# Optimization experiments

Measured on AMD Instinct MI355X. Metric: run time of the kernel, lower is better.

The kernel has to match this reference:

```python
import jax, jax.numpy as jnp
import numpy as np

WAY, SHOT, QUERY = 64, 8, 16


def setup_inputs() -> dict:
    key = jax.random.key(0)
    k1, k2 = jax.random.split(key)
    t, c = 32, 1024
    query_feat = jax.random.normal(k1, (t, WAY * QUERY, c), dtype=jnp.float32)
    support_feat = jax.random.normal(k2, (t, WAY * SHOT, c), dtype=jnp.float32)
    return {"query_feat": query_feat, "support_feat": support_feat}


def reference(query_feat, support_feat):
    t, wq, c = query_feat.shape
    # prototypes: mean over shots -> [t, way, c]
    proto = jnp.mean(support_feat.reshape(t, WAY, SHOT, c), axis=2)
    # squared Euclidean via expansion: ||q||^2 - 2 q.p + ||p||^2
    q_sq = jnp.sum(query_feat * query_feat, axis=-1, keepdims=True)      # [t, wq, 1]
    p_sq = jnp.sum(proto * proto, axis=-1)[:, None, :]                   # [t, 1, way]
    qp = jnp.einsum('tqc,twc->tqw', query_feat, proto)                   # [t, wq, way]
    dist = -(q_sq - 2.0 * qp + p_sq)
    return dist
```

## Files before the change

kernel.cpp:

```cpp
#include <hip/hip_runtime.h>
#include <hip/hip_bf16.h>

#define T 32
#define WAYS 64
#define SHOTS 8
#define CDIM 1024
#define WQ 1024
#define BK 128
#define NK 8

typedef float f32x4 __attribute__((ext_vector_type(4)));
typedef __bf16 bf16x8 __attribute__((ext_vector_type(8)));

__global__ __launch_bounds__(256) void proto_kernel(const float* __restrict__ support,
                                                    __bf16* __restrict__ proto,
                                                    float* __restrict__ p_sq) {
    const int bid = blockIdx.x;
    const int tid = threadIdx.x;
    const float* sp = support + (size_t)bid * (SHOTS * CDIM);
    float4 a = make_float4(0.f, 0.f, 0.f, 0.f);
#pragma unroll
    for (int s = 0; s < SHOTS; ++s) {
        const float4 v = *reinterpret_cast<const float4*>(sp + s * CDIM + tid * 4);
        a.x += v.x; a.y += v.y; a.z += v.z; a.w += v.w;
    }
    a.x *= 0.125f; a.y *= 0.125f; a.z *= 0.125f; a.w *= 0.125f;
    float ps = a.x * a.x + a.y * a.y + a.z * a.z + a.w * a.w;

    union { __bf16 h[4]; uint2 u; } pk;
    pk.h[0] = (__bf16)a.x; pk.h[1] = (__bf16)a.y; pk.h[2] = (__bf16)a.z; pk.h[3] = (__bf16)a.w;
    *reinterpret_cast<uint2*>(proto + (size_t)bid * CDIM + tid * 4) = pk.u;

#pragma unroll
    for (int m = 32; m >= 1; m >>= 1) ps += __shfl_down(ps, m, 64);
    __shared__ float red[4];
    const int wv = tid >> 6, ln = tid & 63;
    if (ln == 0) red[wv] = ps;
    __syncthreads();
    if (tid == 0) p_sq[bid] = red[0] + red[1] + red[2] + red[3];
}

__global__ __launch_bounds__(512, 4) void dist_kernel(const float* __restrict__ query,
                                                      const __bf16* __restrict__ proto,
                                                      const float* __restrict__ p_sq,
                                                      float* __restrict__ out) {
    const int bx = blockIdx.x;
    const int vb = (bx & 7) * 64 + (bx >> 3);
    const int t   = vb >> 4;
    const int mt  = vb & 15;
    const int tid = threadIdx.x;
    const int lane = tid & 63;
    const int wid  = tid >> 6;
    const int wr   = wid >> 1;
    const int wn   = wid & 1;
    const int fr   = lane & 15;
    const int kg   = lane >> 4;

    __shared__ __bf16 As[2][64 * BK];
    __shared__ __bf16 Bs[2][64 * BK];
    __shared__ float qsq_s[64];

    const int srow = tid >> 3;
    const int sk8  = tid & 7;

    const float*  qbase = query + ((size_t)(t * WQ + mt * 64 + srow)) * CDIM + sk8 * 16;
    const __bf16* pbase = proto + ((size_t)(t * WAYS + srow)) * CDIM + sk8 * 16;

    struct Stage { f32x4 a[4]; uint4 b[2]; };

    auto LOAD = [&](int ks) -> Stage {
        Stage s;
        const float* ap = qbase + ks * BK;
#pragma unroll
        for (int p = 0; p < 4; ++p)
            s.a[p] = *reinterpret_cast<const f32x4*>(ap + p * 4);
        const __bf16* bp = pbase + ks * BK;
        s.b[0] = *reinterpret_cast<const uint4*>(bp);
        s.b[1] = *reinterpret_cast<const uint4*>(bp + 8);
        return s;
    };

    float qsq = 0.f;

    auto WRITE = [&](int buf, const Stage& s) {
#pragma unroll
        for (int p = 0; p < 4; ++p)
            qsq += s.a[p].x * s.a[p].x + s.a[p].y * s.a[p].y +
                   s.a[p].z * s.a[p].z + s.a[p].w * s.a[p].w;
        union { __bf16 h[8]; uint4 u; } p0, p1;
#pragma unroll
        for (int j = 0; j < 2; ++j) {
            const f32x4 v0 = s.a[j * 2], v1 = s.a[j * 2 + 1];
            __bf16* h = (j == 0) ? p0.h : p1.h;
            h[0] = (__bf16)v0.x; h[1] = (__bf16)v0.y; h[2] = (__bf16)v0.z; h[3] = (__bf16)v0.w;
            h[4] = (__bf16)v1.x; h[5] = (__bf16)v1.y; h[6] = (__bf16)v1.z; h[7] = (__bf16)v1.w;
        }
        const int swz = (srow & 7) << 4;
        char* ab = reinterpret_cast<char*>(As[buf]);
        *reinterpret_cast<uint4*>(ab + ((srow * 256 + sk8 * 32) ^ swz))      = p0.u;
        *reinterpret_cast<uint4*>(ab + ((srow * 256 + sk8 * 32 + 16) ^ swz)) = p1.u;
        char* bb = reinterpret_cast<char*>(Bs[buf]);
        *reinterpret_cast<uint4*>(bb + ((srow * 256 + sk8 * 32) ^ swz))      = s.b[0];
        *reinterpret_cast<uint4*>(bb + ((srow * 256 + sk8 * 32 + 16) ^ swz)) = s.b[1];
    };

    f32x4 acc[2];
    acc[0] = (f32x4){0.f, 0.f, 0.f, 0.f};
    acc[1] = (f32x4){0.f, 0.f, 0.f, 0.f};

    auto COMPUTE = [&](int buf) {
        const char* ab = reinterpret_cast<const char*>(As[buf]);
        const char* bb = reinterpret_cast<const char*>(Bs[buf]);
#pragma unroll
        for (int ksub = 0; ksub < 4; ++ksub) {
            const int arow = wr * 16 + fr;
            const bf16x8 af = *reinterpret_cast<const bf16x8*>(
                ab + ((arow * 256 + ksub * 64 + kg * 16) ^ ((arow & 7) << 4)));
#pragma unroll
            for (int nf = 0; nf < 2; ++nf) {
                const int way = wn * 32 + nf * 16 + fr;
                const bf16x8 bf = *reinterpret_cast<const bf16x8*>(
                    bb + ((way * 256 + ksub * 64 + kg * 16) ^ ((way & 7) << 4)));
                acc[nf] = __builtin_amdgcn_mfma_f32_16x16x32_bf16(af, bf, acc[nf], 0, 0, 0);
            }
        }
    };

    float psqv[2];
#pragma unroll
    for (int nf = 0; nf < 2; ++nf)
        psqv[nf] = p_sq[t * WAYS + wn * 32 + nf * 16 + fr];

    Stage s0 = LOAD(0);
    Stage sA = LOAD(1);
    WRITE(0, s0);
    asm volatile("s_waitcnt lgkmcnt(0)" ::: "memory");
    __builtin_amdgcn_s_barrier();

#pragma unroll
    for (int ks = 0; ks < NK; ++ks) {
        Stage nx;
        if (ks < NK - 2) nx = LOAD(ks + 2);
        COMPUTE(ks & 1);
        if (ks < NK - 1) WRITE((ks + 1) & 1, sA);
        sA = nx;
        asm volatile("s_waitcnt lgkmcnt(0)" ::: "memory");
        __builtin_amdgcn_s_barrier();
    }

    qsq += __shfl_xor(qsq, 1, 64);
    qsq += __shfl_xor(qsq, 2, 64);
    qsq += __shfl_xor(qsq, 4, 64);
    if (sk8 == 0) qsq_s[srow] = qsq;
    __syncthreads();

    float* ob = out + ((size_t)(t * WQ + mt * 64 + wr * 16)) * WAYS;
#pragma unroll
    for (int r = 0; r < 4; ++r) {
        const int row = kg * 4 + r;
        const float qv = qsq_s[wr * 16 + row];
#pragma unroll
        for (int nf = 0; nf < 2; ++nf) {
            ob[(size_t)row * WAYS + wn * 32 + nf * 16 + fr] =
                2.f * acc[nf][r] - qv - psqv[nf];
        }
    }
}

extern "C" void kernel_launch(void* const* d_in, const int* in_sizes, int n_in,
                              void* d_out, int out_size, void* d_ws, size_t ws_size,
                              hipStream_t stream) {
    const float* query   = (const float*)d_in[0];
    const float* support = (const float*)d_in[1];
    float* out = (float*)d_out;

    __bf16* proto = (__bf16*)d_ws;
    float*  p_sq  = (float*)((char*)d_ws + (size_t)T * WAYS * CDIM * sizeof(__bf16));

    hipLaunchKernelGGL(proto_kernel, dim3(T * WAYS), dim3(256), 0, stream,
                       support, proto, p_sq);
    hipLaunchKernelGGL(dist_kernel, dim3(T * 16), dim3(512), 0, stream,
                       query, proto, p_sq, out);
}
```

Measured before the change: 38.87 us.

## Fuse prototype computation into distance kernel with per-batch atomic counter sync

Merges the prototype-averaging kernel into the distance GEMM kernel. Each of the 16 blocks for a batch index computes 4 prototypes, then bumps an atomic counter. Blocks prefetch their query tiles while tid 0 spins until all 16 producers for that batch have finished. This removes a kernel launch and lets query loads overlap the prototype phase. In exchange it adds a memset and an inter-block spin-wait that relies on all blocks being co-resident; 512 blocks at 4 per CU should fit on the device.

New measurement: 96.22 us. 148% more time.

```diff
diff --git a/kernel.cpp b/kernel.cpp
--- a/kernel.cpp
+++ b/kernel.cpp
@@ -12,38 +12,12 @@
 typedef float f32x4 __attribute__((ext_vector_type(4)));
 typedef __bf16 bf16x8 __attribute__((ext_vector_type(8)));
 
-__global__ __launch_bounds__(256) void proto_kernel(const float* __restrict__ support,
-                                                    __bf16* __restrict__ proto,
-                                                    float* __restrict__ p_sq) {
-    const int bid = blockIdx.x;
-    const int tid = threadIdx.x;
-    const float* sp = support + (size_t)bid * (SHOTS * CDIM);
-    float4 a = make_float4(0.f, 0.f, 0.f, 0.f);
-#pragma unroll
-    for (int s = 0; s < SHOTS; ++s) {
-        const float4 v = *reinterpret_cast<const float4*>(sp + s * CDIM + tid * 4);
-        a.x += v.x; a.y += v.y; a.z += v.z; a.w += v.w;
-    }
-    a.x *= 0.125f; a.y *= 0.125f; a.z *= 0.125f; a.w *= 0.125f;
-    float ps = a.x * a.x + a.y * a.y + a.z * a.z + a.w * a.w;
-
-    union { __bf16 h[4]; uint2 u; } pk;
-    pk.h[0] = (__bf16)a.x; pk.h[1] = (__bf16)a.y; pk.h[2] = (__bf16)a.z; pk.h[3] = (__bf16)a.w;
-    *reinterpret_cast<uint2*>(proto + (size_t)bid * CDIM + tid * 4) = pk.u;
-
-#pragma unroll
-    for (int m = 32; m >= 1; m >>= 1) ps += __shfl_down(ps, m, 64);
-    __shared__ float red[4];
-    const int wv = tid >> 6, ln = tid & 63;
-    if (ln == 0) red[wv] = ps;
-    __syncthreads();
-    if (tid == 0) p_sq[bid] = red[0] + red[1] + red[2] + red[3];
-}
-
-__global__ __launch_bounds__(512, 4) void dist_kernel(const float* __restrict__ query,
-                                                      const __bf16* __restrict__ proto,
-                                                      const float* __restrict__ p_sq,
-                                                      float* __restrict__ out) {
+__global__ __launch_bounds__(512, 4) void fused_kernel(const float* __restrict__ query,
+                                                       const float* __restrict__ support,
+                                                       float* __restrict__ out,
+                                                       __bf16* __restrict__ proto,
+                                                       float* __restrict__ p_sq,
+                                                       int* __restrict__ cnt) {
     const int bx = blockIdx.x;
     const int vb = (bx & 7) * 64 + (bx >> 3);
     const int t   = vb >> 4;
@@ -51,10 +25,49 @@
     const int tid = threadIdx.x;
     const int lane = tid & 63;
     const int wid  = tid >> 6;
-    const int wr   = wid >> 1;
-    const int wn   = wid & 1;
-    const int fr   = lane & 15;
-    const int kg   = lane >> 4;
+
+    __shared__ float redA[8];
+
+    {
+        const int bid = vb * 4 + (wid >> 1);
+        const int ch  = (wid & 1) * 512;
+        const float* sp = support + (size_t)bid * (SHOTS * CDIM) + ch;
+
+        f32x4 a0 = (f32x4){0.f, 0.f, 0.f, 0.f};
+        f32x4 a1 = (f32x4){0.f, 0.f, 0.f, 0.f};
+#pragma unroll
+        for (int s = 0; s < SHOTS; ++s) {
+            a0 += *reinterpret_cast<const f32x4*>(sp + s * CDIM + lane * 4);
+            a1 += *reinterpret_cast<const f32x4*>(sp + s * CDIM + 256 + lane * 4);
+        }
+        a0 *= 0.125f; a1 *= 0.125f;
+        float ps = a0.x * a0.x + a0.y * a0.y + a0.z * a0.z + a0.w * a0.w +
+                   a1.x * a1.x + a1.y * a1.y + a1.z * a1.z + a1.w * a1.w;
+
+        union { __bf16 h[4]; uint2 u; } q0, q1;
+        q0.h[0] = (__bf16)a0.x; q0.h[1] = (__bf16)a0.y;
+        q0.h[2] = (__bf16)a0.z; q0.h[3] = (__bf16)a0.w;
+        q1.h[0] = (__bf16)a1.x; q1.h[1] = (__bf16)a1.y;
+        q1.h[2] = (__bf16)a1.z; q1.h[3] = (__bf16)a1.w;
+        __bf16* pb = proto + (size_t)bid * CDIM + ch;
+        *reinterpret_cast<uint2*>(pb + lane * 4)       = q0.u;
+        *reinterpret_cast<uint2*>(pb + 256 + lane * 4) = q1.u;
+
+#pragma unroll
+        for (int m = 1; m <= 32; m <<= 1) ps += __shfl_xor(ps, m, 64);
+        if (lane == 0) redA[wid] = ps;
+        __syncthreads();
+        if (tid < 4) p_sq[vb * 4 + tid] = redA[2 * tid] + redA[2 * tid + 1];
+        __syncthreads();
+    }
+
+    if (tid == 0)
+        __hip_atomic_fetch_add(&cnt[t], 1, __ATOMIC_RELEASE, __HIP_MEMORY_SCOPE_AGENT);
+
+    const int wr = wid >> 1;
+    const int wn = wid & 1;
+    const int fr = lane & 15;
+    const int kg = lane >> 4;
 
     __shared__ __bf16 As[2][64 * BK];
     __shared__ __bf16 Bs[2][64 * BK];
@@ -66,14 +79,19 @@
     const float*  qbase = query + ((size_t)(t * WQ + mt * 64 + srow)) * CDIM + sk8 * 16;
     const __bf16* pbase = proto + ((size_t)(t * WAYS + srow)) * CDIM + sk8 * 16;
 
-    struct Stage { f32x4 a[4]; uint4 b[2]; };
-
-    auto LOAD = [&](int ks) -> Stage {
-        Stage s;
+    struct StageA { f32x4 a[4]; };
+    struct StageB { uint4 b[2]; };
+
+    auto LOADA = [&](int ks) -> StageA {
+        StageA s;
         const float* ap = qbase + ks * BK;
 #pragma unroll
         for (int p = 0; p < 4; ++p)
             s.a[p] = *reinterpret_cast<const f32x4*>(ap + p * 4);
+        return s;
+    };
+    auto LOADB = [&](int ks) -> StageB {
+        StageB s;
         const __bf16* bp = pbase + ks * BK;
         s.b[0] = *reinterpret_cast<const uint4*>(bp);
         s.b[1] = *reinterpret_cast<const uint4*>(bp + 8);
@@ -82,15 +100,15 @@
 
     float qsq = 0.f;
 
-    auto WRITE = [&](int buf, const Stage& s) {
+    auto WRITE = [&](int buf, const StageA& sa, const StageB& sb) {
 #pragma unroll
         for (int p = 0; p < 4; ++p)
-            qsq += s.a[p].x * s.a[p].x + s.a[p].y * s.a[p].y +
-                   s.a[p].z * s.a[p].z + s.a[p].w * s.a[p].w;
+            qsq += sa.a[p].x * sa.a[p].x + sa.a[p].y * sa.a[p].y +
+                   sa.a[p].z * sa.a[p].z + sa.a[p].w * sa.a[p].w;
         union { __bf16 h[8]; uint4 u; } p0, p1;
 #pragma unroll
         for (int j = 0; j < 2; ++j) {
-            const f32x4 v0 = s.a[j * 2], v1 = s.a[j * 2 + 1];
+            const f32x4 v0 = sa.a[j * 2], v1 = sa.a[j * 2 + 1];
             __bf16* h = (j == 0) ? p0.h : p1.h;
             h[0] = (__bf16)v0.x; h[1] = (__bf16)v0.y; h[2] = (__bf16)v0.z; h[3] = (__bf16)v0.w;
             h[4] = (__bf16)v1.x; h[5] = (__bf16)v1.y; h[6] = (__bf16)v1.z; h[7] = (__bf16)v1.w;
@@ -100,8 +118,8 @@
         *reinterpret_cast<uint4*>(ab + ((srow * 256 + sk8 * 32) ^ swz))      = p0.u;
         *reinterpret_cast<uint4*>(ab + ((srow * 256 + sk8 * 32 + 16) ^ swz)) = p1.u;
         char* bb = reinterpret_cast<char*>(Bs[buf]);
-        *reinterpret_cast<uint4*>(bb + ((srow * 256 + sk8 * 32) ^ swz))      = s.b[0];
-        *reinterpret_cast<uint4*>(bb + ((srow * 256 + sk8 * 32 + 16) ^ swz)) = s.b[1];
+        *reinterpret_cast<uint4*>(bb + ((srow * 256 + sk8 * 32) ^ swz))      = sb.b[0];
+        *reinterpret_cast<uint4*>(bb + ((srow * 256 + sk8 * 32 + 16) ^ swz)) = sb.b[1];
     };
 
     f32x4 acc[2];
@@ -126,24 +144,34 @@
         }
     };
 
+    StageA sa0 = LOADA(0);
+    StageA saA = LOADA(1);
+
+    if (tid == 0) {
+        while (__hip_atomic_load(&cnt[t], __ATOMIC_RELAXED, __HIP_MEMORY_SCOPE_AGENT) < 16)
+            __builtin_amdgcn_s_sleep(8);
+    }
+    __syncthreads();
+    __builtin_amdgcn_fence(__ATOMIC_ACQUIRE, "agent");
+
     float psqv[2];
 #pragma unroll
     for (int nf = 0; nf < 2; ++nf)
         psqv[nf] = p_sq[t * WAYS + wn * 32 + nf * 16 + fr];
 
-    Stage s0 = LOAD(0);
-    Stage sA = LOAD(1);
-    WRITE(0, s0);
+    StageB sb0 = LOADB(0);
+    StageB sbA = LOADB(1);
+    WRITE(0, sa0, sb0);
     asm volatile("s_waitcnt lgkmcnt(0)" ::: "memory");
     __builtin_amdgcn_s_barrier();
 
 #pragma unroll
     for (int ks = 0; ks < NK; ++ks) {
-        Stage nx;
-        if (ks < NK - 2) nx = LOAD(ks + 2);
+        StageA nxa; StageB nxb;
+        if (ks < NK - 2) { nxa = LOADA(ks + 2); nxb = LOADB(ks + 2); }
         COMPUTE(ks & 1);
-        if (ks < NK - 1) WRITE((ks + 1) & 1, sA);
-        sA = nx;
+        if (ks < NK - 1) WRITE((ks + 1) & 1, saA, sbA);
+        saA = nxa; sbA = nxb;
         asm volatile("s_waitcnt lgkmcnt(0)" ::: "memory");
         __builtin_amdgcn_s_barrier();
     }
@@ -174,11 +202,14 @@
     const float* support = (const float*)d_in[1];
     float* out = (float*)d_out;
 
+    const size_t PROTO_BYTES = (size_t)T * WAYS * CDIM * sizeof(__bf16);
+    const size_t PSQ_BYTES   = (size_t)T * WAYS * sizeof(float);
     __bf16* proto = (__bf16*)d_ws;
-    float*  p_sq  = (float*)((char*)d_ws + (size_t)T * WAYS * CDIM * sizeof(__bf16));
-
-    hipLaunchKernelGGL(proto_kernel, dim3(T * WAYS), dim3(256), 0, stream,
-                       support, proto, p_sq);
-    hipLaunchKernelGGL(dist_kernel, dim3(T * 16), dim3(512), 0, stream,
-                       query, proto, p_sq, out);
+    float*  p_sq  = (float*)((char*)d_ws + PROTO_BYTES);
+    int*    cnt   = (int*)((char*)d_ws + PROTO_BYTES + PSQ_BYTES);
+
+    hipMemsetAsync(cnt, 0, T * sizeof(int), stream);
+
+    hipLaunchKernelGGL(fused_kernel, dim3(T * 16), dim3(512), 0, stream,
+                       query, support, out, proto, p_sq, cnt);
 }
```
